# Kernel optimization log

Hardware: AMD Instinct MI355X
Metric: run time of the kernel (lower is better)

## Reference

```python
import jax, jax.numpy as jnp
import numpy as np
from jax import lax


def conv2d(x, w, padding):
    # x: [B,C,H,W], w: [O,I,kh,kw]; torch Conv2d == cross-correlation, same as lax default
    return lax.conv_general_dilated(x, w, (1, 1), padding,
                                    dimension_numbers=('NCHW', 'OIHW', 'NCHW'))


def setup_inputs() -> dict:
    key = jax.random.key(0)
    ks = jax.random.split(key, 16)
    B, C1, C2, H1, W1, H2, W2, ratio = 8, 256, 512, 64, 64, 32, 32, 8
    Cr = C1 // ratio  # 32
    s = 0.05
    return {
        'x1': jax.random.normal(ks[0], (B, C1, H1, W1), jnp.float32),
        'x2': jax.random.normal(ks[1], (B, C2, H2, W2), jnp.float32),
        'wq': jax.random.normal(ks[2], (Cr, C1, 3, 3), jnp.float32) * s,
        'wk': jax.random.normal(ks[3], (Cr, C2, 3, 3), jnp.float32) * s,
        'wv': jax.random.normal(ks[4], (C1, C2, 3, 3), jnp.float32) * s,
        'wc': jax.random.normal(ks[5], (1, C1, 1, 1), jnp.float32) * s,
        'wch': jax.random.normal(ks[6], (C1, C1, 3, 3), jnp.float32) * s,
        'wt1': jax.random.normal(ks[7], (Cr, C1, 1, 1), jnp.float32) * s,
        'bt1': jax.random.normal(ks[8], (Cr,), jnp.float32) * s,
        'ln_g': jnp.ones((Cr, 1, 1), jnp.float32),
        'ln_b': jnp.zeros((Cr, 1, 1), jnp.float32),
        'wt2': jax.random.normal(ks[9], (C1, Cr, 1, 1), jnp.float32) * s,
        'bt2': jax.random.normal(ks[10], (C1,), jnp.float32) * s,
    }


def reference(x1, x2, wq, wk, wv, wc, wch, wt1, bt1, ln_g, ln_b, wt2, bt2):
    B, C1, H1, W1 = x1.shape
    N1 = H1 * W1
    N2 = x2.shape[2] * x2.shape[3]
    eps = 1e-5

    # spatial cross-attention branch
    q = conv2d(x1, wq, 'SAME').reshape(B, -1, N1)          # [B,Cr,N1]
    k = conv2d(x2, wk, 'SAME').reshape(B, -1, N2)          # [B,Cr,N2]
    v = conv2d(x2, wv, 'SAME').reshape(B, C1, N2)          # [B,C1,N2]
    content = jnp.einsum('bcn,bcm->bnm', k, q)             # [B,N2,N1] (key^T @ query)
    content = jax.nn.softmax(content, axis=1)              # softmax over N2 (dim=1)
    att_con = jnp.einsum('bcn,bnm->bcm', v, content).reshape(B, C1, H1, W1) + x1

    # channel attention branch
    cf = conv2d(x1, wc, 'VALID').reshape(B, 1, N1)         # 1x1 conv -> [B,1,N1]
    cf = jax.nn.softmax(cf.transpose(0, 2, 1), axis=1)     # [B,N1,1], softmax over N1
    chf = conv2d(x1, wch, 'SAME').reshape(B, C1, N1)       # [B,C1,N1]
    pool = jnp.einsum('bcn,bno->bco', chf, cf).reshape(B, C1, 1, 1)

    t = conv2d(pool, wt1, 'VALID') + bt1.reshape(1, -1, 1, 1)  # [B,Cr,1,1]
    mu = jnp.mean(t, axis=(1, 2, 3), keepdims=True)
    var = jnp.mean((t - mu) ** 2, axis=(1, 2, 3), keepdims=True)
    t = (t - mu) * lax.rsqrt(var + eps) * ln_g[None] + ln_b[None]
    t = jax.nn.relu(t)
    channel_weight = conv2d(t, wt2, 'VALID') + bt2.reshape(1, -1, 1, 1)  # [B,C1,1,1]

    return att_con + x1 * channel_weight
```

## Files before the change

### kernel.cpp

```cpp
#include <hip/hip_runtime.h>
#include <stdint.h>

#define LL long long

typedef short short8 __attribute__((ext_vector_type(8)));
typedef float f32x4 __attribute__((ext_vector_type(4)));
typedef unsigned int uint2v __attribute__((ext_vector_type(2)));

__device__ __forceinline__ unsigned short f2bf(float f) {
  unsigned u = __float_as_uint(f);
  unsigned r = (u + 0x7fffu + ((u >> 16) & 1u)) >> 16;
  return (unsigned short)r;
}
__device__ __forceinline__ float bf2f(unsigned short h) {
  return __uint_as_float(((unsigned)h) << 16);
}

#define MFMA16(A, B, C) __builtin_amdgcn_mfma_f32_16x16x32_bf16(A, B, C, 0, 0, 0)

__global__ __launch_bounds__(256) void wtrans2(
    const float* __restrict__ src, unsigned short* __restrict__ dh,
    unsigned short* __restrict__ dl, int OC, int IC)
{
  const int i = blockIdx.x * 256 + threadIdx.x;
  if (i >= OC * IC * 9) return;
  const int off = i % 9;
  const int rest = i / 9;
  const int ic = rest % IC;
  const int oc = rest / IC;
  const float v = src[i];
  const unsigned short h = f2bf(v);
  const LL di = (((LL)off * (IC >> 5) + (ic >> 5)) * OC + oc) * 32 + (ic & 31);
  dh[di] = h;
  if (dl) dl[di] = f2bf(v - bf2f(h));
}

__global__ __launch_bounds__(256) void transp(
    const float* __restrict__ src, unsigned short* __restrict__ dh,
    unsigned short* __restrict__ dl, int C, int N)
{
  __shared__ unsigned short sh[64 * 66];
  __shared__ unsigned short sl[64 * 66];
  const int t = threadIdx.x;
  const int b = blockIdx.z;
  const int n0 = blockIdx.x * 64, c0 = blockIdx.y * 64;
  {
    const int nl = t & 63, cl0 = t >> 6;
#pragma unroll
    for (int i = 0; i < 16; ++i) {
      const int cl = cl0 + 4 * i;
      const float v = src[((LL)b * C + c0 + cl) * N + n0 + nl];
      const unsigned short h = f2bf(v);
      sh[nl * 66 + cl] = h;
      sl[nl * 66 + cl] = f2bf(v - bf2f(h));
    }
  }
  __syncthreads();
  {
    const int cl = t & 63, nr0 = t >> 6;
    const int chunk = (c0 + cl) >> 5;
    const int cin = cl & 31;
#pragma unroll
    for (int j = 0; j < 16; ++j) {
      const int nr = nr0 + 4 * j;
      const LL di = (((LL)b * (C >> 5) + chunk) * N + n0 + nr) * 32 + cin;
      dh[di] = sh[nr * 66 + cl];
      if (dl) dl[di] = sl[nr * 66 + cl];
    }
  }
}

template<int NW>
__global__ __launch_bounds__(NW * 64) void conv_qk_s(
    const unsigned short* __restrict__ xh, const unsigned short* __restrict__ xl,
    const unsigned short* __restrict__ wh, const unsigned short* __restrict__ wl,
    unsigned short* __restrict__ dh, unsigned short* __restrict__ dl,
    int logW, int H)
{
  __shared__ float sred[NW][16][64];
  const int t = threadIdx.x, w = t >> 6, lane = t & 63;
  const int lo4 = lane & 15, hi4 = lane >> 4;
  const int b = blockIdx.z;
  const int W = 1 << logW;
  const int N = H * W;
  const int px0 = blockIdx.x * 32;
  const int row = px0 >> logW;
  const int x0 = px0 & (W - 1);
  const int ch = w;
  const short8 zero8 = {0, 0, 0, 0, 0, 0, 0, 0};

  f32x4 acc[2][2];
#pragma unroll
  for (int p = 0; p < 2; ++p)
#pragma unroll
    for (int ot = 0; ot < 2; ++ot) acc[p][ot] = (f32x4){0.f, 0.f, 0.f, 0.f};

  const LL xbase = ((LL)(b * NW + ch)) * N * 32 + hi4 * 8;
#pragma unroll
  for (int ky = 0; ky < 3; ++ky) {
    const int gy = row + ky - 1;
    const bool oky = (unsigned)gy < (unsigned)H;
    const int gyc = min(max(gy, 0), H - 1);
#pragma unroll
    for (int kx = 0; kx < 3; ++kx) {
      short8 Bh[2], Bl[2];
#pragma unroll
      for (int p = 0; p < 2; ++p) {
        const int gx = x0 + p * 16 + lo4 + kx - 1;
        const bool ok = oky && ((unsigned)gx < (unsigned)W);
        const int gxc = min(max(gx, 0), W - 1);
        const LL xoff = xbase + (LL)(gyc * W + gxc) * 32;
        const short8 bh = *(const short8*)(xh + xoff);
        const short8 bl = *(const short8*)(xl + xoff);
        Bh[p] = ok ? bh : zero8;
        Bl[p] = ok ? bl : zero8;
      }
      const int off = ky * 3 + kx;
      short8 Ah[2], Al[2];
#pragma unroll
      for (int ot = 0; ot < 2; ++ot) {
        const LL wi = ((LL)(off * NW + ch) * 32 + ot * 16 + lo4) * 32 + hi4 * 8;
        Ah[ot] = *(const short8*)(wh + wi);
        Al[ot] = *(const short8*)(wl + wi);
      }
#pragma unroll
      for (int p = 0; p < 2; ++p)
#pragma unroll
        for (int ot = 0; ot < 2; ++ot) {
          acc[p][ot] = MFMA16(Ah[ot], Bh[p], acc[p][ot]);
          acc[p][ot] = MFMA16(Ah[ot], Bl[p], acc[p][ot]);
          acc[p][ot] = MFMA16(Al[ot], Bh[p], acc[p][ot]);
        }
    }
  }
#pragma unroll
  for (int p = 0; p < 2; ++p)
#pragma unroll
    for (int ot = 0; ot < 2; ++ot)
#pragma unroll
      for (int r = 0; r < 4; ++r)
        sred[w][p * 8 + ot * 4 + r][lane] = acc[p][ot][r];
  __syncthreads();
  constexpr int SPW = 16 / NW;
#pragma unroll
  for (int si = 0; si < SPW; ++si) {
    const int slot = w * SPW + si;
    float v = sred[0][slot][lane];
#pragma unroll
    for (int j = 1; j < NW; ++j) v += sred[j][slot][lane];
    const int p = slot >> 3, ot = (slot >> 2) & 1, r = slot & 3;
    const LL di = ((LL)b * N + px0 + p * 16 + lo4) * 32 + ot * 16 + hi4 * 4 + r;
    const unsigned short h = f2bf(v);
    dh[di] = h;
    dl[di] = f2bf(v - bf2f(h));
  }
}

__global__ __launch_bounds__(512) void conv_v_w(
    const unsigned short* __restrict__ xh, const unsigned short* __restrict__ wt,
    unsigned short* __restrict__ out)
{
  __shared__ float sred[4][32][64];
  const int t = threadIdx.x, w = t >> 6, lane = t & 63;
  const int lo4 = lane & 15, hi4 = lane >> 4;
  const int b = blockIdx.z;
  const int h = w & 1, ocg = (w >> 1) & 1, kp = w >> 2;
  const int r0 = blockIdx.x * 4;
  const int ocb = blockIdx.y * 64 + ocg * 32;
  const short8 zero8 = {0, 0, 0, 0, 0, 0, 0, 0};

  f32x4 acc[4][2];
#pragma unroll
  for (int rr = 0; rr < 4; ++rr)
#pragma unroll
    for (int ot = 0; ot < 2; ++ot) acc[rr][ot] = (f32x4){0.f, 0.f, 0.f, 0.f};

  for (int ch = kp * 8; ch < kp * 8 + 8; ++ch) {
    short8 A[3][3][2];
#pragma unroll
    for (int ky = 0; ky < 3; ++ky)
#pragma unroll
      for (int kx = 0; kx < 3; ++kx)
#pragma unroll
        for (int ot = 0; ot < 2; ++ot) {
          const int off = ky * 3 + kx;
          A[ky][kx][ot] = *(const short8*)(
              wt + ((LL)(off * 16 + ch) * 256 + ocb + ot * 16 + lo4) * 32 + hi4 * 8);
        }
    const LL xchb = ((LL)(b * 16 + ch)) * 1024 * 32 + hi4 * 8;
#pragma unroll
    for (int g = 0; g < 6; ++g) {
      const int gy = r0 - 1 + g;
      const bool oky = (unsigned)gy < 32u;
      const int gyc = min(max(gy, 0), 31);
      short8 Bg[3];
#pragma unroll
      for (int kx = 0; kx < 3; ++kx) {
        const int gx = h * 16 + lo4 + kx - 1;
        const bool ok = oky && ((unsigned)gx < 32u);
        const int gxc = min(max(gx, 0), 31);
        const short8 bv = *(const short8*)(xh + xchb + (LL)(gyc * 32 + gxc) * 32);
        Bg[kx] = ok ? bv : zero8;
      }
#pragma unroll
      for (int rr = 0; rr < 4; ++rr) {
        if (rr > g || rr + 2 < g) continue;
        const int ky = g - rr;
#pragma unroll
        for (int kx = 0; kx < 3; ++kx)
#pragma unroll
          for (int ot = 0; ot < 2; ++ot)
            acc[rr][ot] = MFMA16(A[ky][kx][ot], Bg[kx], acc[rr][ot]);
      }
    }
  }
  const int slotbase = h * 2 + ocg;
  if (kp == 1) {
#pragma unroll
    for (int rr = 0; rr < 4; ++rr)
#pragma unroll
      for (int ot = 0; ot < 2; ++ot)
#pragma unroll
        for (int r = 0; r < 4; ++r)
          sred[slotbase][rr * 8 + ot * 4 + r][lane] = acc[rr][ot][r];
  }
  __syncthreads();
  if (kp == 0) {
#pragma unroll
    for (int rr = 0; rr < 4; ++rr)
#pragma unroll
      for (int ot = 0; ot < 2; ++ot)
#pragma unroll
        for (int r = 0; r < 4; ++r) {
          const float v = acc[rr][ot][r] + sred[slotbase][rr * 8 + ot * 4 + r][lane];
          const int row = r0 + rr;
          const int oc = ocb + ot * 16 + hi4 * 4 + r;
          out[(((LL)b * 32 + row) * 256 + oc) * 32 + h * 16 + lo4] = f2bf(v);
        }
  }
}

__global__ __launch_bounds__(256) void cf_dot(
    const float* __restrict__ x1, const float* __restrict__ wc, float* __restrict__ cf)
{
  const int b = blockIdx.y;
  const int n = blockIdx.x * 256 + threadIdx.x;
  const float* xp = x1 + (LL)b * 256 * 4096 + n;
  float a = 0.f;
#pragma unroll 4
  for (int c = 0; c < 256; ++c)
    a = fmaf(xp[(LL)c * 4096], wc[c], a);
  cf[b * 4096 + n] = a;
}

__global__ __launch_bounds__(1024) void cf_softmax(
    const float* __restrict__ cf, float* __restrict__ cfs)
{
  const int b = blockIdx.x, t = threadIdx.x;
  __shared__ float r1[16];
  __shared__ float r2[16];
  float v[4];
#pragma unroll
  for (int j = 0; j < 4; ++j) v[j] = cf[b * 4096 + t + 1024 * j];
  float mx = fmaxf(fmaxf(v[0], v[1]), fmaxf(v[2], v[3]));
#pragma unroll
  for (int k = 1; k <= 32; k <<= 1) mx = fmaxf(mx, __shfl_xor(mx, k));
  const int wv = t >> 6;
  if ((t & 63) == 0) r1[wv] = mx;
  __syncthreads();
  float m2 = r1[0];
#pragma unroll
  for (int i = 1; i < 16; ++i) m2 = fmaxf(m2, r1[i]);
  float e[4]; float s = 0.f;
#pragma unroll
  for (int j = 0; j < 4; ++j) { e[j] = __expf(v[j] - m2); s += e[j]; }
#pragma unroll
  for (int k = 1; k <= 32; k <<= 1) s += __shfl_xor(s, k);
  if ((t & 63) == 0) r2[wv] = s;
  __syncthreads();
  float s2 = 0.f;
#pragma unroll
  for (int i = 0; i < 16; ++i) s2 += r2[i];
  const float inv = 1.f / s2;
#pragma unroll
  for (int j = 0; j < 4; ++j) cfs[b * 4096 + t + 1024 * j] = e[j] * inv;
}

__global__ __launch_bounds__(256) void ykern(
    const float* __restrict__ x1, const float* __restrict__ cfs, float* __restrict__ T)
{
  __shared__ float cl[6][64];
  const int chunk = blockIdx.x, b = blockIdx.y, t = threadIdx.x;
  for (int idx = t; idx < 384; idx += 256) {
    int lr = idx >> 6, col = idx & 63;
    int gr = chunk * 4 - 1 + lr;
    cl[lr][col] = ((unsigned)gr < 64u) ? cfs[b * 4096 + gr * 64 + col] : 0.f;
  }
  __syncthreads();
  const int c = t;
  float a[9];
#pragma unroll
  for (int k = 0; k < 9; ++k) a[k] = 0.f;
  const float* xp = x1 + ((LL)b * 256 + c) * 4096 + chunk * 256;
  for (int i = 0; i < 256; ++i) {
    float xv = xp[i];
    int yl = i >> 6, col = i & 63;
#pragma unroll
    for (int dy = 0; dy < 3; ++dy) {
      int lr = yl + 2 - dy;
#pragma unroll
      for (int dx = 0; dx < 3; ++dx) {
        int cc = col + 1 - dx;
        float f = ((unsigned)cc < 64u) ? cl[lr][cc] : 0.f;
        a[dy * 3 + dx] = fmaf(xv, f, a[dy * 3 + dx]);
      }
    }
  }
#pragma unroll
  for (int k = 0; k < 9; ++k)
    atomicAdd(&T[((LL)b * 256 + c) * 9 + k], a[k]);
}

__global__ __launch_bounds__(256) void pool_k(
    const float* __restrict__ T, const float* __restrict__ wch,
    float* __restrict__ pool)
{
  __shared__ __align__(16) float Tl[2304];
  const int b = blockIdx.y, ocg = blockIdx.x;
  const int t = threadIdx.x, w = t >> 6, lane = t & 63;
  for (int i = t; i < 2304; i += 256) Tl[i] = T[(LL)b * 2304 + i];
  __syncthreads();
  const float4* tp = (const float4*)Tl;
#pragma unroll
  for (int oi = 0; oi < 2; ++oi) {
    const int oc = ocg * 8 + w * 2 + oi;
    const float4* wp = (const float4*)(wch + (LL)oc * 2304);
    float a = 0.f;
#pragma unroll
    for (int j = 0; j < 9; ++j) {
      const int idx = lane + 64 * j;
      float4 w4 = wp[idx], t4 = tp[idx];
      a = fmaf(w4.x, t4.x, a); a = fmaf(w4.y, t4.y, a);
      a = fmaf(w4.z, t4.z, a); a = fmaf(w4.w, t4.w, a);
    }
#pragma unroll
    for (int k = 1; k <= 32; k <<= 1) a += __shfl_xor(a, k);
    if (lane == 0) pool[b * 256 + oc] = a;
  }
}

__global__ __launch_bounds__(256) void chw_tail(
    const float* __restrict__ pool_g,
    const float* __restrict__ wt1, const float* __restrict__ bt1,
    const float* __restrict__ lng, const float* __restrict__ lnb,
    const float* __restrict__ wt2, const float* __restrict__ bt2,
    float* __restrict__ cwp1)
{
  const int b = blockIdx.x, t = threadIdx.x;
  __shared__ float pool[256];
  __shared__ float tt[32];
  pool[t] = pool_g[b * 256 + t];
  __syncthreads();
  if (t < 64) {
    float tv = 0.f;
    if (t < 32) {
      const float* wp = wt1 + (LL)t * 256;
      for (int c = 0; c < 256; ++c) tv = fmaf(wp[c], pool[c], tv);
      tv += bt1[t];
    }
    float s = tv;
#pragma unroll
    for (int k = 1; k <= 16; k <<= 1) s += __shfl_xor(s, k);
    float mu = s * (1.f / 32.f);
    float d = tv - mu;
    float vs = d * d;
#pragma unroll
    for (int k = 1; k <= 16; k <<= 1) vs += __shfl_xor(vs, k);
    float var = vs * (1.f / 32.f);
    if (t < 32) {
      float nrm = d / sqrtf(var + 1e-5f);
      float y = nrm * lng[t] + lnb[t];
      tt[t] = fmaxf(y, 0.f);
    }
  }
  __syncthreads();
  {
    float s2 = bt2[t];
    const float* wp = wt2 + (LL)t * 32;
#pragma unroll
    for (int i = 0; i < 32; ++i) s2 = fmaf(wp[i], tt[i], s2);
    cwp1[b * 256 + t] = 1.f + s2;
  }
}

__global__ __launch_bounds__(256) void attn_stats(
    const unsigned short* __restrict__ qh_g, const unsigned short* __restrict__ ql_g,
    const unsigned short* __restrict__ kh_g, const unsigned short* __restrict__ kl_g,
    float* __restrict__ mxs, float* __restrict__ invl)
{
  const int t = threadIdx.x, w = t >> 6, lane = t & 63;
  const int lo4 = lane & 15, hi4 = lane >> 4;
  const int b = blockIdx.y, mc = blockIdx.x * 64;
  const float L2E = 1.4426950408889634f;

  short8 qh[4], ql[4];
#pragma unroll
  for (int mt = 0; mt < 4; ++mt) {
    const LL qa = ((LL)(b * 4096 + mc + mt * 16 + lo4)) * 32 + hi4 * 8;
    qh[mt] = *(const short8*)(qh_g + qa);
    ql[mt] = *(const short8*)(ql_g + qa);
  }

  float M[4], L[4];
#pragma unroll
  for (int mt = 0; mt < 4; ++mt) { M[mt] = -1e30f; L[mt] = 0.f; }

  for (int ns = 0; ns < 16; ++ns) {
    const int n = w * 256 + ns * 16 + lo4;
    const LL ka = ((LL)(b * 1024 + n)) * 32 + hi4 * 8;
    const short8 kh = *(const short8*)(kh_g + ka);
    const short8 kl = *(const short8*)(kl_g + ka);
#pragma unroll
    for (int mt = 0; mt < 4; ++mt) {
      f32x4 s = {0.f, 0.f, 0.f, 0.f};
      s = MFMA16(kl, qh[mt], s);
      s = MFMA16(kh, ql[mt], s);
      s = MFMA16(kh, qh[mt], s);
      float lm = fmaxf(fmaxf(s[0], s[1]), fmaxf(s[2], s[3]));
      float nM = fmaxf(M[mt], lm);
      float sc = exp2f((M[mt] - nM) * L2E);
      L[mt] = L[mt] * sc + exp2f((s[0] - nM) * L2E) + exp2f((s[1] - nM) * L2E)
                         + exp2f((s[2] - nM) * L2E) + exp2f((s[3] - nM) * L2E);
      M[mt] = nM;
    }
  }
#pragma unroll
  for (int mask = 16; mask <= 32; mask <<= 1) {
#pragma unroll
    for (int mt = 0; mt < 4; ++mt) {
      float oM = __shfl_xor(M[mt], mask), oL = __shfl_xor(L[mt], mask);
      float nM = fmaxf(M[mt], oM);
      L[mt] = L[mt] * exp2f((M[mt] - nM) * L2E) + oL * exp2f((oM - nM) * L2E);
      M[mt] = nM;
    }
  }
  __shared__ float sM[4][64], sL[4][64];
  if (lane < 16) {
#pragma unroll
    for (int mt = 0; mt < 4; ++mt) {
      sM[w][mt * 16 + lane] = M[mt];
      sL[w][mt * 16 + lane] = L[mt];
    }
  }
  __syncthreads();
  if (t < 64) {
    float Mg = sM[0][t], Lg = sL[0][t];
#pragma unroll
    for (int wv = 1; wv < 4; ++wv) {
      float oM = sM[wv][t], oL = sL[wv][t];
      float nM = fmaxf(Mg, oM);
      Lg = Lg * exp2f((Mg - nM) * L2E) + oL * exp2f((oM - nM) * L2E);
      Mg = nM;
    }
    mxs[b * 4096 + mc + t] = Mg * L2E;
    invl[b * 4096 + mc + t] = 1.f / Lg;
  }
}

__global__ __launch_bounds__(256) void attn_pv(
    const unsigned short* __restrict__ qh_g, const unsigned short* __restrict__ ql_g,
    const unsigned short* __restrict__ kh_g, const unsigned short* __restrict__ kl_g,
    const unsigned short* __restrict__ v16,
    const float* __restrict__ mxs, const float* __restrict__ invl,
    const float* __restrict__ x1, const float* __restrict__ cwp1,
    float* __restrict__ out)
{
  __shared__ __align__(16) unsigned short Pt[2][32][136];
  const int t = threadIdx.x, w = t >> 6, lane = t & 63;
  const int lo4 = lane & 15, hi4 = lane >> 4;
  const int b = blockIdx.y, mb = blockIdx.x * 32;
  const float L2E = 1.4426950408889634f;

  short8 qh[2], ql[2];
  float mxv[2], ilv[2];
#pragma unroll
  for (int mt = 0; mt < 2; ++mt) {
    const int m = mb + mt * 16 + lo4;
    const LL qa = ((LL)(b * 4096 + m)) * 32 + hi4 * 8;
    qh[mt] = *(const short8*)(qh_g + qa);
    ql[mt] = *(const short8*)(ql_g + qa);
    mxv[mt] = mxs[b * 4096 + m];
    ilv[mt] = invl[b * 4096 + m];
  }

  f32x4 acc[4][2];
#pragma unroll
  for (int ct = 0; ct < 4; ++ct)
#pragma unroll
    for (int mt = 0; mt < 2; ++mt) acc[ct][mt] = (f32x4){0.f, 0.f, 0.f, 0.f};

  short8 kh[2], kl[2];
#pragma unroll
  for (int ns = 0; ns < 2; ++ns) {
    const LL ka = ((LL)(b * 1024 + w * 32 + ns * 16 + lo4)) * 32 + hi4 * 8;
    kh[ns] = *(const short8*)(kh_g + ka);
    kl[ns] = *(const short8*)(kl_g + ka);
  }

  int buf = 0;
  for (int nt = 0; nt < 8; ++nt) {
    short8 knh[2], knl[2];
    {
      const int ntn = (nt + 1) & 7;
#pragma unroll
      for (int ns = 0; ns < 2; ++ns) {
        const LL ka = ((LL)(b * 1024 + ntn * 128 + w * 32 + ns * 16 + lo4)) * 32 + hi4 * 8;
        knh[ns] = *(const short8*)(kh_g + ka);
        knl[ns] = *(const short8*)(kl_g + ka);
      }
    }
    f32x4 s[2][2];
#pragma unroll
    for (int ns = 0; ns < 2; ++ns)
#pragma unroll
      for (int mt = 0; mt < 2; ++mt) {
        f32x4 z = {0.f, 0.f, 0.f, 0.f};
        z = MFMA16(kl[ns], qh[mt], z);
        z = MFMA16(kh[ns], ql[mt], z);
        z = MFMA16(kh[ns], qh[mt], z);
        s[ns][mt] = z;
      }
    short8 vpre[2][4];
#pragma unroll
    for (int ks = 0; ks < 2; ++ks)
#pragma unroll
      for (int ct = 0; ct < 4; ++ct)
        vpre[ks][ct] = *(const short8*)(
            v16 + (((LL)b * 32 + nt * 4 + ks) * 256 + w * 64 + ct * 16 + lo4) * 32 + hi4 * 8);
#pragma unroll
    for (int ns = 0; ns < 2; ++ns)
#pragma unroll
      for (int mt = 0; mt < 2; ++mt) {
        const int m_loc = mt * 16 + lo4;
        const int nl = w * 32 + ns * 16 + hi4 * 4;
        float p0 = exp2f(fmaf(s[ns][mt][0], L2E, -mxv[mt])) * ilv[mt];
        float p1 = exp2f(fmaf(s[ns][mt][1], L2E, -mxv[mt])) * ilv[mt];
        float p2 = exp2f(fmaf(s[ns][mt][2], L2E, -mxv[mt])) * ilv[mt];
        float p3 = exp2f(fmaf(s[ns][mt][3], L2E, -mxv[mt])) * ilv[mt];
        uint2v u;
        u[0] = (unsigned)f2bf(p0) | ((unsigned)f2bf(p1) << 16);
        u[1] = (unsigned)f2bf(p2) | ((unsigned)f2bf(p3) << 16);
        *(uint2v*)&Pt[buf][m_loc][nl] = u;
      }
    __syncthreads();
#pragma unroll
    for (int ks = 0; ks < 4; ++ks) {
      short8 pb[2];
#pragma unroll
      for (int mt = 0; mt < 2; ++mt)
        pb[mt] = *(const short8*)&Pt[buf][mt * 16 + lo4][ks * 32 + hi4 * 8];
#pragma unroll
      for (int ct = 0; ct < 4; ++ct) {
        const short8 va = (ks < 2)
            ? vpre[ks][ct]
            : *(const short8*)(
                  v16 + (((LL)b * 32 + nt * 4 + ks) * 256 + w * 64 + ct * 16 + lo4) * 32 + hi4 * 8);
#pragma unroll
        for (int mt = 0; mt < 2; ++mt)
          acc[ct][mt] = MFMA16(va, pb[mt], acc[ct][mt]);
      }
    }
    buf ^= 1;
#pragma unroll
    for (int ns = 0; ns < 2; ++ns) { kh[ns] = knh[ns]; kl[ns] = knl[ns]; }
  }

#pragma unroll
  for (int ct = 0; ct < 4; ++ct)
#pragma unroll
    for (int mt = 0; mt < 2; ++mt) {
      const int m = mb + mt * 16 + lo4;
#pragma unroll
      for (int r = 0; r < 4; ++r) {
        const int c = w * 64 + ct * 16 + hi4 * 4 + r;
        const float cw = cwp1[b * 256 + c];
        const LL off = ((LL)(b * 256 + c)) * 4096 + m;
        out[off] = acc[ct][mt][r] + x1[off] * cw;
      }
    }
}

extern "C" void kernel_launch(void* const* d_in, const int* in_sizes, int n_in,
                              void* d_out, int out_size, void* d_ws, size_t ws_size,
                              hipStream_t stream) {
  const float* x1  = (const float*)d_in[0];
  const float* x2  = (const float*)d_in[1];
  const float* wq  = (const float*)d_in[2];
  const float* wk  = (const float*)d_in[3];
  const float* wv  = (const float*)d_in[4];
  const float* wc  = (const float*)d_in[5];
  const float* wch = (const float*)d_in[6];
  const float* wt1 = (const float*)d_in[7];
  const float* bt1 = (const float*)d_in[8];
  const float* lng = (const float*)d_in[9];
  const float* lnb = (const float*)d_in[10];
  const float* wt2 = (const float*)d_in[11];
  const float* bt2 = (const float*)d_in[12];
  float* outp = (float*)d_out;

  float* ws   = (float*)d_ws;
  float* qtf  = ws;
  float* ktf  = qtf + 1048576;
  float* mxsb = ktf + 262144;
  float* invb = mxsb + 32768;
  float* cfr  = invb + 32768;
  float* cfs  = cfr + 32768;
  float* Tb   = cfs + 32768;
  float* cwb  = Tb + 18432;
  unsigned short* sbase = (unsigned short*)(cwb + 2048);
  unsigned short* v16  = sbase;
  unsigned short* x1th = v16  + 2097152;
  unsigned short* x1tl = x1th + 8388608;
  unsigned short* x2th = x1tl + 8388608;
  unsigned short* x2tl = x2th + 4194304;
  unsigned short* wvt  = x2tl + 4194304;
  unsigned short* wqh  = wvt  + 1179648;
  unsigned short* wql  = wqh  + 73728;
  unsigned short* wkh  = wql  + 73728;
  unsigned short* wkl  = wkh  + 147456;

  unsigned short* qhg = (unsigned short*)qtf;
  unsigned short* qlg = qhg + 1048576;
  unsigned short* khg = (unsigned short*)ktf;
  unsigned short* klg = khg + 262144;

  hipMemsetAsync(Tb, 0, (size_t)18432 * 4, stream);

  wtrans2<<<dim3(4608), 256, 0, stream>>>(wv, wvt, nullptr, 256, 512);
  wtrans2<<<dim3(288),  256, 0, stream>>>(wq, wqh, wql, 32, 256);
  wtrans2<<<dim3(576),  256, 0, stream>>>(wk, wkh, wkl, 32, 512);

  transp<<<dim3(64, 4, 8), 256, 0, stream>>>(x1, x1th, x1tl, 256, 4096);
  transp<<<dim3(16, 8, 8), 256, 0, stream>>>(x2, x2th, x2tl, 512, 1024);

  conv_qk_s<16><<<dim3(32, 1, 8), 1024, 0, stream>>>(
      x2th, x2tl, wkh, wkl, khg, klg, 5, 32);

  conv_v_w<<<dim3(8, 4, 8), 512, 0, stream>>>(x2th, wvt, v16);

  conv_qk_s<8><<<dim3(128, 1, 8), 512, 0, stream>>>(
      x1th, x1tl, wqh, wql, qhg, qlg, 6, 64);

  cf_dot<<<dim3(16, 8), 256, 0, stream>>>(x1, wc, cfr);
  cf_softmax<<<dim3(8), 1024, 0, stream>>>(cfr, cfs);
  ykern<<<dim3(16, 8), 256, 0, stream>>>(x1, cfs, Tb);
  pool_k<<<dim3(32, 8), 256, 0, stream>>>(Tb, wch, cfr);
  chw_tail<<<dim3(8), 256, 0, stream>>>(cfr, wt1, bt1, lng, lnb, wt2, bt2, cwb);

  attn_stats<<<dim3(64, 8), 256, 0, stream>>>(qhg, qlg, khg, klg, mxsb, invb);
  attn_pv<<<dim3(128, 8), 256, 0, stream>>>(qhg, qlg, khg, klg, v16, mxsb, invb, x1, cwb, outp);
}
```

Before: 417.9 us.

## Restructure channel pooling correlation into per-row-pair partials with separate reduction

Replaces the ykern kernel, which looped serially over 256 pixels per thread and then combined results with atomics, with ykern2. In ykern2 each thread holds one full image row in registers and uses float4 row-filter loads from shared memory. Two rows per block are combined in shared memory, and per-block partials are written to scratch space that reuses the x2 transposed buffer. A new red_t kernel sums those partials, which removes both the memset and the atomicAdds. Grid parallelism doubles and global loads are vectorized, at the cost of one extra launch, the scratch traffic, and relying on x2th being dead at that point.

```diff
diff --git a/kernel.cpp b/kernel.cpp
--- a/kernel.cpp
+++ b/kernel.cpp
@@ -286,39 +286,74 @@
   for (int j = 0; j < 4; ++j) cfs[b * 4096 + t + 1024 * j] = e[j] * inv;
 }
 
-__global__ __launch_bounds__(256) void ykern(
-    const float* __restrict__ x1, const float* __restrict__ cfs, float* __restrict__ T)
-{
-  __shared__ float cl[6][64];
-  const int chunk = blockIdx.x, b = blockIdx.y, t = threadIdx.x;
-  for (int idx = t; idx < 384; idx += 256) {
-    int lr = idx >> 6, col = idx & 63;
-    int gr = chunk * 4 - 1 + lr;
-    cl[lr][col] = ((unsigned)gr < 64u) ? cfs[b * 4096 + gr * 64 + col] : 0.f;
-  }
-  __syncthreads();
-  const int c = t;
+__global__ __launch_bounds__(512) void ykern2(
+    const float* __restrict__ x1, const float* __restrict__ cfs,
+    float* __restrict__ ykp)
+{
+  __shared__ __align__(16) float cl2[64][4];
+  __shared__ float sredY[256][9];
+  const int t = threadIdx.x;
+  const int c = t & 255, h = t >> 8;
+  const int bx = blockIdx.x, b = blockIdx.y;
+  const int base = bx * 2;
+  if (t < 256) {
+    const int r = t >> 6, cc = t & 63;
+    const int grow = base - 1 + r;
+    cl2[cc][r] = ((unsigned)grow < 64u) ? cfs[b * 4096 + grow * 64 + cc] : 0.f;
+  }
+  __syncthreads();
+  const int row = base + h;
+  float xr[66];
+  xr[0] = 0.f; xr[65] = 0.f;
+  {
+    const float4* xp = (const float4*)(x1 + ((LL)(b * 256 + c)) * 4096 + row * 64);
+#pragma unroll
+    for (int j = 0; j < 16; ++j) {
+      const float4 v = xp[j];
+      xr[1 + 4 * j] = v.x; xr[2 + 4 * j] = v.y;
+      xr[3 + 4 * j] = v.z; xr[4 + 4 * j] = v.w;
+    }
+  }
   float a[9];
 #pragma unroll
   for (int k = 0; k < 9; ++k) a[k] = 0.f;
-  const float* xp = x1 + ((LL)b * 256 + c) * 4096 + chunk * 256;
-  for (int i = 0; i < 256; ++i) {
-    float xv = xp[i];
-    int yl = i >> 6, col = i & 63;
-#pragma unroll
-    for (int dy = 0; dy < 3; ++dy) {
-      int lr = yl + 2 - dy;
-#pragma unroll
-      for (int dx = 0; dx < 3; ++dx) {
-        int cc = col + 1 - dx;
-        float f = ((unsigned)cc < 64u) ? cl[lr][cc] : 0.f;
-        a[dy * 3 + dx] = fmaf(xv, f, a[dy * 3 + dx]);
-      }
-    }
-  }
-#pragma unroll
-  for (int k = 0; k < 9; ++k)
-    atomicAdd(&T[((LL)b * 256 + c) * 9 + k], a[k]);
+  const bool h1 = (h == 1);
+#pragma unroll
+  for (int c0 = 0; c0 < 64; ++c0) {
+    const float4 f4 = *(const float4*)&cl2[c0][0];
+    const float f_dy0 = h1 ? f4.w : f4.z;
+    const float f_dy1 = h1 ? f4.z : f4.y;
+    const float f_dy2 = h1 ? f4.y : f4.x;
+#pragma unroll
+    for (int dx = 0; dx < 3; ++dx) {
+      const float xv = xr[c0 + dx];
+      a[0 * 3 + dx] = fmaf(xv, f_dy0, a[0 * 3 + dx]);
+      a[1 * 3 + dx] = fmaf(xv, f_dy1, a[1 * 3 + dx]);
+      a[2 * 3 + dx] = fmaf(xv, f_dy2, a[2 * 3 + dx]);
+    }
+  }
+  if (h1) {
+#pragma unroll
+    for (int k = 0; k < 9; ++k) sredY[c][k] = a[k];
+  }
+  __syncthreads();
+  if (!h1) {
+    float* op = ykp + ((LL)(b * 32 + bx)) * 2304 + c * 9;
+#pragma unroll
+    for (int k = 0; k < 9; ++k) op[k] = a[k] + sredY[c][k];
+  }
+}
+
+__global__ __launch_bounds__(256) void red_t(
+    const float* __restrict__ src, float* __restrict__ dst)
+{
+  const int b = blockIdx.y;
+  const int i = blockIdx.x * 256 + threadIdx.x;
+  if (i >= 576) return;
+  const f32x4* sp = (const f32x4*)(src + (LL)b * 32 * 2304);
+  f32x4 a = sp[i];
+  for (int p = 1; p < 32; ++p) a += sp[p * 576 + i];
+  ((f32x4*)(dst + (LL)b * 2304))[i] = a;
 }
 
 __global__ __launch_bounds__(256) void pool_k(
@@ -634,7 +669,7 @@
   unsigned short* khg = (unsigned short*)ktf;
   unsigned short* klg = khg + 262144;
 
-  hipMemsetAsync(Tb, 0, (size_t)18432 * 4, stream);
+  float* ykp = (float*)x2th;
 
   wtrans2<<<dim3(4608), 256, 0, stream>>>(wv, wvt, nullptr, 256, 512);
   wtrans2<<<dim3(288),  256, 0, stream>>>(wq, wqh, wql, 32, 256);
@@ -653,7 +688,8 @@
 
   cf_dot<<<dim3(16, 8), 256, 0, stream>>>(x1, wc, cfr);
   cf_softmax<<<dim3(8), 1024, 0, stream>>>(cfr, cfs);
-  ykern<<<dim3(16, 8), 256, 0, stream>>>(x1, cfs, Tb);
+  ykern2<<<dim3(32, 8), 512, 0, stream>>>(x1, cfs, ykp);
+  red_t<<<dim3(3, 8), 256, 0, stream>>>(ykp, Tb);
   pool_k<<<dim3(32, 8), 256, 0, stream>>>(Tb, wch, cfr);
   chw_tail<<<dim3(8), 256, 0, stream>>>(cfr, wt1, bt1, lng, lnb, wt2, bt2, cwb);
 
```

New measurement: 375.5 us. 1.11x faster.
